# Kernel optimization log

Hardware: AMD Instinct MI355X
Metric: run time of the kernel (lower is better)

Reference implementation:

```python
import jax, jax.numpy as jnp
import numpy as np

EPS = 1e-6

def rmsnorm(x, w):
    rms = jnp.sqrt(jnp.mean(x * x, axis=-1, keepdims=True) + EPS)
    return w * x / rms

def setup_inputs() -> dict:
    key = jax.random.key(0)
    ks = jax.random.split(key, 12)
    B, L, D, S, E, H = 2, 2048, 1024, 16, 4, 2048
    x = jax.random.normal(ks[0], (B, L, D), jnp.float32)
    A_log = jnp.log(jax.random.uniform(ks[1], (D, S), jnp.float32) * 0.5 + 0.5)
    D_param = jnp.ones((D,), jnp.float32)
    W_delta = jax.random.normal(ks[2], (D, D), jnp.float32) * 0.02
    b_delta = jnp.zeros((D,), jnp.float32)
    W_B = jax.random.normal(ks[3], (D, S), jnp.float32) * 0.02
    W_C = jax.random.normal(ks[4], (D, S), jnp.float32) * 0.02
    W_router = jax.random.normal(ks[5], (D, E), jnp.float32) * 0.02
    Wg = jax.random.normal(ks[6], (E, D, H), jnp.float32) * 0.02
    Wu = jax.random.normal(ks[7], (E, D, H), jnp.float32) * 0.02
    Wd = jax.random.normal(ks[8], (E, H, D), jnp.float32) * 0.02
    wn_exp = jnp.ones((E, H), jnp.float32)
    norm_w = jnp.ones((D,), jnp.float32)
    return dict(x=x, A_log=A_log, D_param=D_param, W_delta=W_delta, b_delta=b_delta,
                W_B=W_B, W_C=W_C, W_router=W_router, Wg=Wg, Wu=Wu, Wd=Wd,
                wn_exp=wn_exp, norm_w=norm_w)

def reference(x, A_log, D_param, W_delta, b_delta, W_B, W_C, W_router, Wg, Wu, Wd, wn_exp, norm_w):
    B, L, D = x.shape
    # input-dependent SSM parameters
    delta = jax.nn.softplus(x @ W_delta + b_delta)        # (B,L,D)
    Bm = x @ W_B                                          # (B,L,S)
    Cm = x @ W_C                                          # (B,L,S)
    A = -jnp.exp(A_log)                                   # (D,S)
    S = A.shape[1]
    h0 = jnp.zeros((B, D, S), x.dtype)
    xs = (jnp.moveaxis(x, 1, 0), jnp.moveaxis(delta, 1, 0),
          jnp.moveaxis(Bm, 1, 0), jnp.moveaxis(Cm, 1, 0))

    def step(h, inp):
        x_t, d_t, B_t, C_t = inp                          # (B,D),(B,D),(B,S),(B,S)
        bar_A = jnp.exp(jnp.minimum(d_t[..., None] * A, 10.0))          # (B,D,S)
        bar_B = jnp.clip(d_t[..., None] * B_t[:, None, :], -10.0, 10.0)  # (B,D,S)
        h = jnp.clip(bar_A * h + bar_B * x_t[..., None], -10000.0, 10000.0)
        y_t = jnp.sum(h * C_t[:, None, :], axis=-1) + x_t * D_param     # (B,D)
        return h, y_t

    _, ys = jax.lax.scan(step, h0, xs)                    # ys: (L,B,D)
    ssm_out = jnp.moveaxis(ys, 0, 1)                      # (B,L,D)

    # top-2 MoE over flattened tokens
    flat = ssm_out.reshape(-1, D)                         # (N,D)
    probs = jax.nn.softmax(flat @ W_router, axis=-1)      # (N,E)
    w2, idx2 = jax.lax.top_k(probs, 2)
    w2 = w2 / (jnp.sum(w2, axis=-1, keepdims=True) + 1e-9)

    def expert(xf, wg, wu, wd, wn):
        g = jax.nn.silu(xf @ wg) * (xf @ wu)
        g = rmsnorm(g, wn)
        return g @ wd

    all_out = jax.vmap(expert, in_axes=(None, 0, 0, 0, 0))(flat, Wg, Wu, Wd, wn_exp)  # (E,N,D)
    tok = jnp.arange(flat.shape[0])
    moe = (w2[:, 0, None] * all_out[idx2[:, 0], tok]
           + w2[:, 1, None] * all_out[idx2[:, 1], tok])   # (N,D)

    out = rmsnorm(ssm_out + moe.reshape(B, L, D), norm_w)
    return out  # dropout is identity in eval mode
```

## Files before the change

### kernel.cpp

```cpp
#include <hip/hip_runtime.h>
#include <hip/hip_bf16.h>


typedef __bf16 bfrag __attribute__((ext_vector_type(8)));
typedef float f32x4 __attribute__((ext_vector_type(4)));

constexpr int Ddim = 1024;
constexpr int Sdim = 16;
constexpr int Eexp = 4;
constexpr int Hdim = 2048;
constexpr int Lseq = 2048;
constexpr int Bb   = 2;
constexpr int Ntok = 4096;
constexpr int NC   = 32;
constexpr int CL   = 64;
constexpr int DG   = 64;

__device__ __forceinline__ float softplus_f(float z) {
  return z > 20.f ? z : log1pf(__expf(z));
}

__device__ __forceinline__ bfrag cvt8(float4 a, float4 b) {
  bfrag r;
  r[0] = (__bf16)a.x; r[1] = (__bf16)a.y; r[2] = (__bf16)a.z; r[3] = (__bf16)a.w;
  r[4] = (__bf16)b.x; r[5] = (__bf16)b.y; r[6] = (__bf16)b.z; r[7] = (__bf16)b.w;
  return r;
}

__device__ __forceinline__ void cvt8_split(float4 a, float4 b, bfrag& h, bfrag& l) {
  float v[8] = {a.x, a.y, a.z, a.w, b.x, b.y, b.z, b.w};
  #pragma unroll
  for (int k = 0; k < 8; k++) {
    __bf16 hh = (__bf16)v[k];
    h[k] = hh;
    l[k] = (__bf16)(v[k] - (float)hh);
  }
}

__global__ __launch_bounds__(256) void tr_cvt(const float* __restrict__ src,
                                              __bf16* __restrict__ dst,
                                              int R, int C) {
  __shared__ float tile[32][33];
  const size_t boff = (size_t)blockIdx.z * R * C;
  const int c0 = blockIdx.x * 32, r0 = blockIdx.y * 32;
  const int tx = threadIdx.x & 31, ty = threadIdx.x >> 5;
  #pragma unroll
  for (int i = 0; i < 4; i++)
    tile[ty + 8 * i][tx] = src[boff + (size_t)(r0 + ty + 8 * i) * C + c0 + tx];
  __syncthreads();
  #pragma unroll
  for (int i = 0; i < 4; i++)
    dst[boff + (size_t)(c0 + ty + 8 * i) * R + r0 + tx] = (__bf16)tile[tx][ty + 8 * i];
}

__global__ __launch_bounds__(256) void tr_split(const float* __restrict__ src,
                                                __bf16* __restrict__ dhi,
                                                __bf16* __restrict__ dlo,
                                                int R, int C) {
  __shared__ float tile[32][33];
  const size_t boff = (size_t)blockIdx.z * R * C;
  const int c0 = blockIdx.x * 32, r0 = blockIdx.y * 32;
  const int tx = threadIdx.x & 31, ty = threadIdx.x >> 5;
  #pragma unroll
  for (int i = 0; i < 4; i++)
    tile[ty + 8 * i][tx] = src[boff + (size_t)(r0 + ty + 8 * i) * C + c0 + tx];
  __syncthreads();
  #pragma unroll
  for (int i = 0; i < 4; i++) {
    float v = tile[tx][ty + 8 * i];
    __bf16 h = (__bf16)v;
    size_t idx = boff + (size_t)(c0 + ty + 8 * i) * R + r0 + tx;
    dhi[idx] = h;
    dlo[idx] = (__bf16)(v - (float)h);
  }
}

__global__ __launch_bounds__(256) void gemm_delta(
    const float* __restrict__ Amat, const __bf16* __restrict__ Bhi,
    const __bf16* __restrict__ Blo, const float* __restrict__ bias,
    float* __restrict__ outp) {
  const int n0 = blockIdx.x * 128;
  const int m0 = blockIdx.y * 128;
  const int t = threadIdx.x;
  const int lane = t & 63;
  const int w = t >> 6;
  const int wm = w >> 1, wn = w & 1;
  const int lr = lane & 15, kq = lane >> 4;
  const int ar = t >> 1;
  const int ac = (t & 1) * 16;

  __shared__ __attribute__((aligned(16))) __bf16 Ah[128 * 48];
  __shared__ __attribute__((aligned(16))) __bf16 Alo[128 * 48];
  __shared__ __attribute__((aligned(16))) __bf16 Bh[128 * 48];
  __shared__ __attribute__((aligned(16))) __bf16 Bl[128 * 48];

  f32x4 acc[4][4];
  const f32x4 z4 = {0.f, 0.f, 0.f, 0.f};
  #pragma unroll
  for (int i = 0; i < 4; i++)
    #pragma unroll
    for (int j = 0; j < 4; j++) acc[i][j] = z4;

  const float* Asrc = Amat + (size_t)(m0 + ar) * Ddim + ac;
  const __bf16* Bhsrc = Bhi + (size_t)(n0 + ar) * Ddim + ac;
  const __bf16* Blsrc = Blo + (size_t)(n0 + ar) * Ddim + ac;

  for (int k0 = 0; k0 < Ddim; k0 += 32) {
    __syncthreads();
    {
      float4 f0 = *(const float4*)(Asrc + k0);
      float4 f1 = *(const float4*)(Asrc + k0 + 4);
      float4 f2 = *(const float4*)(Asrc + k0 + 8);
      float4 f3 = *(const float4*)(Asrc + k0 + 12);
      bfrag h0, l0, h1, l1;
      cvt8_split(f0, f1, h0, l0);
      cvt8_split(f2, f3, h1, l1);
      *(bfrag*)&Ah[ar * 48 + ac] = h0;
      *(bfrag*)&Ah[ar * 48 + ac + 8] = h1;
      *(bfrag*)&Alo[ar * 48 + ac] = l0;
      *(bfrag*)&Alo[ar * 48 + ac + 8] = l1;
      *(bfrag*)&Bh[ar * 48 + ac] = *(const bfrag*)(Bhsrc + k0);
      *(bfrag*)&Bh[ar * 48 + ac + 8] = *(const bfrag*)(Bhsrc + k0 + 8);
      *(bfrag*)&Bl[ar * 48 + ac] = *(const bfrag*)(Blsrc + k0);
      *(bfrag*)&Bl[ar * 48 + ac + 8] = *(const bfrag*)(Blsrc + k0 + 8);
    }
    __syncthreads();
    bfrag ah[4], al_[4], bh[4], bl[4];
    #pragma unroll
    for (int i = 0; i < 4; i++) {
      const int off = (wm * 64 + i * 16 + lr) * 48 + kq * 8;
      ah[i] = *(const bfrag*)&Ah[off];
      al_[i] = *(const bfrag*)&Alo[off];
    }
    #pragma unroll
    for (int j = 0; j < 4; j++) {
      const int off = (wn * 64 + j * 16 + lr) * 48 + kq * 8;
      bh[j] = *(const bfrag*)&Bh[off];
      bl[j] = *(const bfrag*)&Bl[off];
    }
    #pragma unroll
    for (int i = 0; i < 4; i++)
      #pragma unroll
      for (int j = 0; j < 4; j++) {
        f32x4 tacc = acc[i][j];
        tacc = __builtin_amdgcn_mfma_f32_16x16x32_bf16(al_[i], bl[j], tacc, 0, 0, 0);
        tacc = __builtin_amdgcn_mfma_f32_16x16x32_bf16(ah[i], bl[j], tacc, 0, 0, 0);
        tacc = __builtin_amdgcn_mfma_f32_16x16x32_bf16(al_[i], bh[j], tacc, 0, 0, 0);
        tacc = __builtin_amdgcn_mfma_f32_16x16x32_bf16(ah[i], bh[j], tacc, 0, 0, 0);
        acc[i][j] = tacc;
      }
  }
  #pragma unroll
  for (int i = 0; i < 4; i++)
    #pragma unroll
    for (int rr = 0; rr < 4; rr++) {
      const int row = m0 + wm * 64 + i * 16 + kq * 4 + rr;
      #pragma unroll
      for (int j = 0; j < 4; j++) {
        const int col = n0 + wn * 64 + j * 16 + lr;
        float zv = acc[i][j][rr] + bias[col];
        outp[(size_t)row * Ddim + col] = softplus_f(zv);
      }
    }
}

__global__ __launch_bounds__(256) void bc_proj(
    const float* __restrict__ x, const float* __restrict__ WB,
    const float* __restrict__ WC, float* __restrict__ Bm, float* __restrict__ Cm) {
  const int n = blockIdx.x * 4 + (threadIdx.x >> 6);
  const int lane = threadIdx.x & 63;
  const int o = lane & 31;
  const int half = lane >> 5;
  const int oc = o & 15;
  const float* W = (o < 16) ? WB : WC;
  const float* xr = x + (size_t)n * Ddim + half * 512;
  const float* Wp = W + (size_t)(half * 512) * Sdim + oc;
  float s = 0.f;
  #pragma unroll 8
  for (int k = 0; k < 512; k++) s += xr[k] * Wp[(size_t)k * Sdim];
  s += __shfl_xor(s, 32);
  if (half == 0) {
    if (o < 16) Bm[(size_t)n * Sdim + oc] = s;
    else        Cm[(size_t)n * Sdim + oc] = s;
  }
}

__global__ __launch_bounds__(1024) void scan_pass1(
    const float* __restrict__ delta, const float* __restrict__ x,
    const float* __restrict__ Bm, const float* __restrict__ A_log,
    float* __restrict__ Ac, float* __restrict__ Bc) {
  const int b = blockIdx.z, c = blockIdx.y, d0 = blockIdx.x * DG;
  const int tid = threadIdx.x;
  const int dl = tid >> 4, s = tid & 15;
  __shared__ __attribute__((aligned(16))) float ld[CL * DG];
  __shared__ __attribute__((aligned(16))) float lx[CL * DG];
  __shared__ __attribute__((aligned(16))) float lb[CL * 16];
  const int t0 = c * CL;
  {
    const int ti = tid >> 4, di = (tid & 15) * 4;
    const size_t src = ((size_t)(b * Lseq + t0 + ti)) * Ddim + d0 + di;
    *(float4*)&ld[ti * DG + di] = *(const float4*)&delta[src];
    *(float4*)&lx[ti * DG + di] = *(const float4*)&x[src];
    if (tid < 256) {
      const int tj = tid >> 2, sj = (tid & 3) * 4;
      *(float4*)&lb[tj * 16 + sj] =
          *(const float4*)&Bm[((size_t)(b * Lseq + t0 + tj)) * Sdim + sj];
    }
  }
  const float A = -__expf(A_log[(d0 + dl) * Sdim + s]);
  __syncthreads();
  float P = 1.f, S = 0.f;
  #pragma unroll 4
  for (int i = 0; i < CL; i++) {
    float dt = ld[i * DG + dl];
    float xt = lx[i * DG + dl];
    float Bt = lb[i * 16 + s];
    float a = __expf(fminf(dt * A, 10.f));
    float bb = fminf(fmaxf(dt * Bt, -10.f), 10.f);
    S = a * S + bb * xt;
    P *= a;
  }
  const size_t o = ((size_t)(b * NC + c) * Ddim + d0 + dl) * Sdim + s;
  Ac[o] = P;
  Bc[o] = S;
}

__global__ __launch_bounds__(256) void scan_pass2(float* __restrict__ Ac,
                                                  const float* __restrict__ Bc) {
  const int idx = blockIdx.x * 256 + threadIdx.x;
  const int b = idx >> 14, r = idx & 16383;
  const size_t base = (size_t)b * (NC * 16384) + r;
  float h = 0.f;
  #pragma unroll 4
  for (int c = 0; c < NC; c++) {
    const size_t a_idx = base + (size_t)c * 16384;
    float a = Ac[a_idx];
    float bb = Bc[a_idx];
    Ac[a_idx] = h;
    h = fmaf(a, h, bb);
  }
}

__global__ __launch_bounds__(1024) void scan_pass3(
    const float* __restrict__ delta, const float* __restrict__ x,
    const float* __restrict__ Bm, const float* __restrict__ Cm,
    const float* __restrict__ A_log, const float* __restrict__ Dp,
    const float* __restrict__ hstart, float* __restrict__ ssm) {
  const int b = blockIdx.z, c = blockIdx.y, d0 = blockIdx.x * DG;
  const int tid = threadIdx.x;
  const int dl = tid >> 4, s = tid & 15;
  __shared__ __attribute__((aligned(16))) float ld[CL * DG];
  __shared__ __attribute__((aligned(16))) float lx[CL * DG];
  __shared__ __attribute__((aligned(16))) float lb[CL * 16];
  __shared__ __attribute__((aligned(16))) float lc[CL * 16];
  __shared__ __attribute__((aligned(16))) float ly[CL * DG];
  const int t0 = c * CL;
  {
    const int ti = tid >> 4, di = (tid & 15) * 4;
    const size_t src = ((size_t)(b * Lseq + t0 + ti)) * Ddim + d0 + di;
    *(float4*)&ld[ti * DG + di] = *(const float4*)&delta[src];
    *(float4*)&lx[ti * DG + di] = *(const float4*)&x[src];
    if (tid < 256) {
      const int tj = tid >> 2, sj = (tid & 3) * 4;
      *(float4*)&lb[tj * 16 + sj] =
          *(const float4*)&Bm[((size_t)(b * Lseq + t0 + tj)) * Sdim + sj];
    } else if (tid < 512) {
      const int u = tid - 256;
      const int tj = u >> 2, sj = (u & 3) * 4;
      *(float4*)&lc[tj * 16 + sj] =
          *(const float4*)&Cm[((size_t)(b * Lseq + t0 + tj)) * Sdim + sj];
    }
  }
  const float A = -__expf(A_log[(d0 + dl) * Sdim + s]);
  const float Dpar = Dp[d0 + dl];
  float h = hstart[((size_t)(b * NC + c) * Ddim + d0 + dl) * Sdim + s];
  __syncthreads();
  #pragma unroll 2
  for (int i = 0; i < CL; i++) {
    float dt = ld[i * DG + dl];
    float xt = lx[i * DG + dl];
    float Bt = lb[i * 16 + s];
    float Ct = lc[i * 16 + s];
    float a = __expf(fminf(dt * A, 10.f));
    float bb = fminf(fmaxf(dt * Bt, -10.f), 10.f);
    h = a * h + bb * xt;
    float yp = h * Ct;
    yp += __shfl_xor(yp, 1);
    yp += __shfl_xor(yp, 2);
    yp += __shfl_xor(yp, 4);
    yp += __shfl_xor(yp, 8);
    if (s == 0) ly[i * DG + dl] = yp + xt * Dpar;
  }
  __syncthreads();
  {
    const int ti = tid >> 4, di = (tid & 15) * 4;
    *(float4*)&ssm[((size_t)(b * Lseq + t0 + ti)) * Ddim + d0 + di] =
        *(const float4*)&ly[ti * DG + di];
  }
}

__global__ __launch_bounds__(256) void router_k(
    const float* __restrict__ ssm, const float* __restrict__ Wr,
    int* __restrict__ counts, int* __restrict__ slotTok,
    int* __restrict__ tokSlot, float* __restrict__ tokW) {
  const int n = blockIdx.x * 4 + (threadIdx.x >> 6);
  const int lane = threadIdx.x & 63;
  const float* xr = ssm + (size_t)n * Ddim;
  float p0 = 0.f, p1 = 0.f, p2 = 0.f, p3 = 0.f;
  for (int k = lane; k < Ddim; k += 64) {
    float xv = xr[k];
    float4 wr = *(const float4*)&Wr[k * 4];
    p0 += xv * wr.x; p1 += xv * wr.y; p2 += xv * wr.z; p3 += xv * wr.w;
  }
  #pragma unroll
  for (int o = 32; o > 0; o >>= 1) {
    p0 += __shfl_xor(p0, o);
    p1 += __shfl_xor(p1, o);
    p2 += __shfl_xor(p2, o);
    p3 += __shfl_xor(p3, o);
  }
  if (lane == 0) {
    float l[4] = {p0, p1, p2, p3};
    float mx = fmaxf(fmaxf(l[0], l[1]), fmaxf(l[2], l[3]));
    float pe[4]; float sum = 0.f;
    #pragma unroll
    for (int e = 0; e < 4; e++) { pe[e] = __expf(l[e] - mx); sum += pe[e]; }
    int i0 = 0;
    #pragma unroll
    for (int e = 1; e < 4; e++) if (pe[e] > pe[i0]) i0 = e;
    int i1 = (i0 == 0) ? 1 : 0;
    #pragma unroll
    for (int e = 0; e < 4; e++) if (e != i0 && e != i1 && pe[e] > pe[i1]) i1 = e;
    float w0 = pe[i0] / sum, w1 = pe[i1] / sum;
    float dn = w0 + w1 + 1e-9f;
    w0 /= dn; w1 /= dn;
    int s0 = atomicAdd(&counts[i0], 1);
    slotTok[i0 * Ntok + s0] = n;
    tokSlot[2 * n] = i0 * Ntok + s0;
    tokW[2 * n] = w0;
    int s1 = atomicAdd(&counts[i1], 1);
    slotTok[i1 * Ntok + s1] = n;
    tokSlot[2 * n + 1] = i1 * Ntok + s1;
    tokW[2 * n + 1] = w1;
  }
}

__global__ void offs_k(const int* __restrict__ counts, int* __restrict__ offs) {
  if (threadIdx.x == 0 && blockIdx.x == 0) {
    int a = 0;
    for (int e = 0; e < Eexp; e++) { offs[e] = a; a += counts[e]; }
    offs[Eexp] = a;
  }
}

__global__ __launch_bounds__(256) void gemm_gateup(
    const float* __restrict__ ssm, const __bf16* __restrict__ WgT,
    const __bf16* __restrict__ WuT, const int* __restrict__ slotTok,
    const int* __restrict__ counts, const int* __restrict__ offs,
    __bf16* __restrict__ g) {
  const int e = blockIdx.z;
  const int cnt = counts[e];
  const int r0 = blockIdx.y * 128;
  if (r0 >= cnt) return;
  const int n0 = blockIdx.x * 128;
  const int t = threadIdx.x;
  const int lane = t & 63;
  const int w = t >> 6;
  const int wm = w >> 1, wn = w & 1;
  const int lr = lane & 15, kq = lane >> 4;
  const int ar = t >> 1;
  const int ac = (t & 1) * 16;

  __shared__ __attribute__((aligned(16))) __bf16 Al[128 * 48];
  __shared__ __attribute__((aligned(16))) __bf16 Bgl[128 * 48];
  __shared__ __attribute__((aligned(16))) __bf16 Bul[128 * 48];

  f32x4 accG[4][4], accU[4][4];
  const f32x4 z4 = {0.f, 0.f, 0.f, 0.f};
  #pragma unroll
  for (int i = 0; i < 4; i++)
    #pragma unroll
    for (int j = 0; j < 4; j++) { accG[i][j] = z4; accU[i][j] = z4; }

  const int rA = r0 + ar;
  const bool valid = rA < cnt;
  const int tok = valid ? slotTok[e * Ntok + rA] : 0;
  const float* Asrc = ssm + (size_t)tok * Ddim + ac;
  const __bf16* Bgsrc = WgT + (size_t)e * Hdim * Ddim + (size_t)(n0 + ar) * Ddim + ac;
  const __bf16* Busrc = WuT + (size_t)e * Hdim * Ddim + (size_t)(n0 + ar) * Ddim + ac;

  for (int k0 = 0; k0 < Ddim; k0 += 32) {
    __syncthreads();
    {
      bfrag v0, v1;
      if (valid) {
        float4 f0 = *(const float4*)(Asrc + k0);
        float4 f1 = *(const float4*)(Asrc + k0 + 4);
        float4 f2 = *(const float4*)(Asrc + k0 + 8);
        float4 f3 = *(const float4*)(Asrc + k0 + 12);
        v0 = cvt8(f0, f1);
        v1 = cvt8(f2, f3);
      } else {
        #pragma unroll
        for (int k = 0; k < 8; k++) { v0[k] = (__bf16)0.f; v1[k] = (__bf16)0.f; }
      }
      *(bfrag*)&Al[ar * 48 + ac] = v0;
      *(bfrag*)&Al[ar * 48 + ac + 8] = v1;
      *(bfrag*)&Bgl[ar * 48 + ac] = *(const bfrag*)(Bgsrc + k0);
      *(bfrag*)&Bgl[ar * 48 + ac + 8] = *(const bfrag*)(Bgsrc + k0 + 8);
      *(bfrag*)&Bul[ar * 48 + ac] = *(const bfrag*)(Busrc + k0);
      *(bfrag*)&Bul[ar * 48 + ac + 8] = *(const bfrag*)(Busrc + k0 + 8);
    }
    __syncthreads();
    bfrag af[4], bg[4], bu[4];
    #pragma unroll
    for (int i = 0; i < 4; i++) af[i] = *(const bfrag*)&Al[(wm * 64 + i * 16 + lr) * 48 + kq * 8];
    #pragma unroll
    for (int j = 0; j < 4; j++) {
      const int off = (wn * 64 + j * 16 + lr) * 48 + kq * 8;
      bg[j] = *(const bfrag*)&Bgl[off];
      bu[j] = *(const bfrag*)&Bul[off];
    }
    #pragma unroll
    for (int i = 0; i < 4; i++)
      #pragma unroll
      for (int j = 0; j < 4; j++) {
        accG[i][j] = __builtin_amdgcn_mfma_f32_16x16x32_bf16(af[i], bg[j], accG[i][j], 0, 0, 0);
        accU[i][j] = __builtin_amdgcn_mfma_f32_16x16x32_bf16(af[i], bu[j], accU[i][j], 0, 0, 0);
      }
  }
  const int gb = offs[e];
  #pragma unroll
  for (int i = 0; i < 4; i++)
    #pragma unroll
    for (int rr = 0; rr < 4; rr++) {
      const int r = r0 + wm * 64 + i * 16 + kq * 4 + rr;
      if (r < cnt) {
        const size_t base = (size_t)(gb + r) * Hdim + n0 + wn * 64 + lr;
        #pragma unroll
        for (int j = 0; j < 4; j++) {
          float zg = accG[i][j][rr];
          float zu = accU[i][j][rr];
          float val = zg / (1.f + __expf(-zg)) * zu;
          g[base + j * 16] = (__bf16)val;
        }
      }
    }
}

__global__ __launch_bounds__(256) void rms_g(__bf16* __restrict__ g,
                                             const float* __restrict__ wn,
                                             const int* __restrict__ offs) {
  const int gs = blockIdx.x;
  const int e = (gs >= offs[1]) + (gs >= offs[2]) + (gs >= offs[3]);
  __bf16* row = g + (size_t)gs * Hdim;
  const int t = threadIdx.x;
  bfrag v = *(const bfrag*)&row[t * 8];
  float f[8]; float ss = 0.f;
  #pragma unroll
  for (int k = 0; k < 8; k++) { f[k] = (float)v[k]; ss += f[k] * f[k]; }
  #pragma unroll
  for (int o = 32; o > 0; o >>= 1) ss += __shfl_xor(ss, o);
  __shared__ float red[4];
  if ((t & 63) == 0) red[t >> 6] = ss;
  __syncthreads();
  float tot = red[0] + red[1] + red[2] + red[3];
  float rinv = 1.f / sqrtf(tot * (1.f / Hdim) + 1e-6f);
  const float* wrow = wn + (size_t)e * Hdim + t * 8;
  bfrag o8;
  #pragma unroll
  for (int k = 0; k < 8; k++) o8[k] = (__bf16)(wrow[k] * f[k] * rinv);
  *(bfrag*)&row[t * 8] = o8;
}

__global__ __launch_bounds__(256) void gemm_down(
    const __bf16* __restrict__ g, const __bf16* __restrict__ WdT,
    const int* __restrict__ counts, const int* __restrict__ offs,
    float* __restrict__ dout) {
  const int e = blockIdx.z;
  const int cnt = counts[e];
  const int r0 = blockIdx.y * 128;
  if (r0 >= cnt) return;
  const int n0 = blockIdx.x * 128;
  const int t = threadIdx.x;
  const int lane = t & 63;
  const int w = t >> 6;
  const int wm = w >> 1, wn = w & 1;
  const int lr = lane & 15, kq = lane >> 4;
  const int ar = t >> 1;
  const int ac = (t & 1) * 16;

  __shared__ __attribute__((aligned(16))) __bf16 Al[128 * 48];
  __shared__ __attribute__((aligned(16))) __bf16 Bl[128 * 48];

  f32x4 acc[4][4];
  const f32x4 z4 = {0.f, 0.f, 0.f, 0.f};
  #pragma unroll
  for (int i = 0; i < 4; i++)
    #pragma unroll
    for (int j = 0; j < 4; j++) acc[i][j] = z4;

  const int rA = r0 + ar;
  const bool valid = rA < cnt;
  const __bf16* Asrc = g + ((size_t)offs[e] + (valid ? rA : 0)) * Hdim + ac;
  const __bf16* Bsrc = WdT + (size_t)e * Ddim * Hdim + (size_t)(n0 + ar) * Hdim + ac;

  for (int k0 = 0; k0 < Hdim; k0 += 32) {
    __syncthreads();
    *(bfrag*)&Al[ar * 48 + ac] = *(const bfrag*)(Asrc + k0);
    *(bfrag*)&Al[ar * 48 + ac + 8] = *(const bfrag*)(Asrc + k0 + 8);
    *(bfrag*)&Bl[ar * 48 + ac] = *(const bfrag*)(Bsrc + k0);
    *(bfrag*)&Bl[ar * 48 + ac + 8] = *(const bfrag*)(Bsrc + k0 + 8);
    __syncthreads();
    bfrag af[4], bf_[4];
    #pragma unroll
    for (int i = 0; i < 4; i++) af[i] = *(const bfrag*)&Al[(wm * 64 + i * 16 + lr) * 48 + kq * 8];
    #pragma unroll
    for (int j = 0; j < 4; j++) bf_[j] = *(const bfrag*)&Bl[(wn * 64 + j * 16 + lr) * 48 + kq * 8];
    #pragma unroll
    for (int i = 0; i < 4; i++)
      #pragma unroll
      for (int j = 0; j < 4; j++)
        acc[i][j] = __builtin_amdgcn_mfma_f32_16x16x32_bf16(af[i], bf_[j], acc[i][j], 0, 0, 0);
  }
  const int gb = offs[e];
  #pragma unroll
  for (int i = 0; i < 4; i++)
    #pragma unroll
    for (int rr = 0; rr < 4; rr++) {
      const int r = r0 + wm * 64 + i * 16 + kq * 4 + rr;
      if (r < cnt) {
        const size_t base = (size_t)(gb + r) * Ddim + n0 + wn * 64 + lr;
        #pragma unroll
        for (int j = 0; j < 4; j++)
          dout[base + j * 16] = acc[i][j][rr];
      }
    }
}

__global__ __launch_bounds__(256) void final_norm(
    const float* __restrict__ ssm, const float* __restrict__ dout,
    const int* __restrict__ tokSlot, const float* __restrict__ tokW,
    const int* __restrict__ offs, const float* __restrict__ nw,
    float* __restrict__ outp) {
  const int n = blockIdx.x;
  const int t = threadIdx.x;
  __shared__ int rows[2];
  __shared__ float ws[2];
  if (t < 2) {
    int pk = tokSlot[2 * n + t];
    rows[t] = offs[pk >> 12] + (pk & (Ntok - 1));
    ws[t] = tokW[2 * n + t];
  }
  __syncthreads();
  const int r0 = rows[0], r1 = rows[1];
  const float w0 = ws[0], w1 = ws[1];
  const size_t base = (size_t)n * Ddim + t * 4;
  float4 a = *(const float4*)&ssm[base];
  float4 m0 = *(const float4*)&dout[(size_t)r0 * Ddim + t * 4];
  float4 m1 = *(const float4*)&dout[(size_t)r1 * Ddim + t * 4];
  float v0 = a.x + w0 * m0.x + w1 * m1.x;
  float v1 = a.y + w0 * m0.y + w1 * m1.y;
  float v2 = a.z + w0 * m0.z + w1 * m1.z;
  float v3 = a.w + w0 * m0.w + w1 * m1.w;
  float ss = v0 * v0 + v1 * v1 + v2 * v2 + v3 * v3;
  #pragma unroll
  for (int o = 32; o > 0; o >>= 1) ss += __shfl_xor(ss, o);
  __shared__ float red[4];
  if ((t & 63) == 0) red[t >> 6] = ss;
  __syncthreads();
  float tot = red[0] + red[1] + red[2] + red[3];
  float rinv = 1.f / sqrtf(tot * (1.f / Ddim) + 1e-6f);
  float4 wv = *(const float4*)&nw[t * 4];
  float4 r;
  r.x = wv.x * v0 * rinv;
  r.y = wv.y * v1 * rinv;
  r.z = wv.z * v2 * rinv;
  r.w = wv.w * v3 * rinv;
  *(float4*)&outp[base] = r;
}

extern "C" void kernel_launch(void* const* d_in, const int* in_sizes, int n_in,
                              void* d_out, int out_size, void* d_ws, size_t ws_size,
                              hipStream_t stream) {
  (void)in_sizes; (void)n_in; (void)out_size; (void)ws_size;
  const float* x        = (const float*)d_in[0];
  const float* A_log    = (const float*)d_in[1];
  const float* D_param  = (const float*)d_in[2];
  const float* W_delta  = (const float*)d_in[3];
  const float* b_delta  = (const float*)d_in[4];
  const float* W_B      = (const float*)d_in[5];
  const float* W_C      = (const float*)d_in[6];
  const float* W_router = (const float*)d_in[7];
  const float* Wg       = (const float*)d_in[8];
  const float* Wu       = (const float*)d_in[9];
  const float* Wd       = (const float*)d_in[10];
  const float* wn_exp   = (const float*)d_in[11];
  const float* norm_w   = (const float*)d_in[12];
  float* out = (float*)d_out;

  char* p = (char*)d_ws;
  auto carve = [&](size_t bytes) -> void* {
    void* r = (void*)p;
    p += (bytes + 255) & ~(size_t)255;
    return r;
  };
  float*  delta   = (float*)  carve((size_t)Ntok * Ddim * 4);
  float*  Ac      = (float*)  carve((size_t)Bb * NC * Ddim * Sdim * 4);
  float*  Bc      = (float*)  carve((size_t)Bb * NC * Ddim * Sdim * 4);
  __bf16* WdT_hi  = (__bf16*) carve((size_t)Ddim * Ddim * 2);
  __bf16* WdT_lo  = (__bf16*) carve((size_t)Ddim * Ddim * 2);
  __bf16* WgT     = (__bf16*) carve((size_t)Eexp * Hdim * Ddim * 2);
  float*  dout    = delta;
  __bf16* WuT     = (__bf16*) carve((size_t)Eexp * Hdim * Ddim * 2);
  __bf16* WdnT    = (__bf16*) carve((size_t)Eexp * Ddim * Hdim * 2);
  float*  Bm      = (float*)  carve((size_t)Ntok * Sdim * 4);
  float*  Cm      = (float*)  carve((size_t)Ntok * Sdim * 4);
  float*  ssm     = (float*)  carve((size_t)Ntok * Ddim * 4);
  __bf16* gbuf    = (__bf16*) carve((size_t)2 * Ntok * Hdim * 2);
  int*    counts  = (int*)    carve(64);
  int*    offs    = (int*)    carve(64);
  int*    slotTok = (int*)    carve((size_t)Eexp * Ntok * 4);
  int*    tokSlot = (int*)    carve((size_t)2 * Ntok * 4);
  float*  tokW    = (float*)  carve((size_t)2 * Ntok * 4);

  hipMemsetAsync(counts, 0, 64, stream);

  tr_split<<<dim3(Ddim / 32, Ddim / 32, 1), 256, 0, stream>>>(W_delta, WdT_hi, WdT_lo, Ddim, Ddim);
  tr_cvt<<<dim3(Hdim / 32, Ddim / 32, Eexp), 256, 0, stream>>>(Wg, WgT, Ddim, Hdim);
  tr_cvt<<<dim3(Hdim / 32, Ddim / 32, Eexp), 256, 0, stream>>>(Wu, WuT, Ddim, Hdim);
  tr_cvt<<<dim3(Ddim / 32, Hdim / 32, Eexp), 256, 0, stream>>>(Wd, WdnT, Hdim, Ddim);

  gemm_delta<<<dim3(Ddim / 128, Ntok / 128), 256, 0, stream>>>(x, WdT_hi, WdT_lo, b_delta, delta);
  bc_proj<<<Ntok / 4, 256, 0, stream>>>(x, W_B, W_C, Bm, Cm);

  scan_pass1<<<dim3(Ddim / DG, NC, Bb), 1024, 0, stream>>>(delta, x, Bm, A_log, Ac, Bc);
  scan_pass2<<<Bb * Ddim * Sdim / 256, 256, 0, stream>>>(Ac, Bc);
  scan_pass3<<<dim3(Ddim / DG, NC, Bb), 1024, 0, stream>>>(delta, x, Bm, Cm, A_log, D_param, Ac, ssm);

  router_k<<<Ntok / 4, 256, 0, stream>>>(ssm, W_router, counts, slotTok, tokSlot, tokW);
  offs_k<<<1, 64, 0, stream>>>(counts, offs);
  gemm_gateup<<<dim3(Hdim / 128, Ntok / 128, Eexp), 256, 0, stream>>>(ssm, WgT, WuT, slotTok, counts, offs, gbuf);
  rms_g<<<2 * Ntok, 256, 0, stream>>>(gbuf, wn_exp, offs);
  gemm_down<<<dim3(Ddim / 128, Ntok / 128, Eexp), 256, 0, stream>>>(gbuf, WdnT, counts, offs, dout);
  final_norm<<<Ntok, 256, 0, stream>>>(ssm, dout, tokSlot, tokW, offs, norm_w, out);
}
```

Measured before the change: 795.1 us.

## Pre-convert GEMM activations to bf16 and stage tiles with direct global-to-LDS loads

Three MFMA GEMMs (delta projection, expert gate/up, expert down) now fill shared memory with global_load_lds 16-byte transfers instead of loading into registers and storing to LDS. To make that possible, new elementwise kernels convert x (into hi/lo bf16 parts) and the SSM output to bf16 ahead of time, so the GEMMs no longer convert fp32 inside their inner loops. Scratch buffers (Ac, gbuf, delta) are reused to hold the converted data. The unpadded 32-element LDS rows may cause bank conflicts on the fragment reads, and the extra conversion passes add memory traffic.

```diff
diff --git a/kernel.cpp b/kernel.cpp
--- a/kernel.cpp
+++ b/kernel.cpp
@@ -37,6 +37,12 @@
   }
 }
 
+__device__ __forceinline__ void gload16(const void* g, void* l) {
+  __builtin_amdgcn_global_load_lds(
+      (const __attribute__((address_space(1))) void*)g,
+      (__attribute__((address_space(3))) void*)l, 16, 0, 0);
+}
+
 __global__ __launch_bounds__(256) void tr_cvt(const float* __restrict__ src,
                                               __bf16* __restrict__ dst,
                                               int R, int C) {
@@ -75,10 +81,30 @@
   }
 }
 
+__global__ __launch_bounds__(256) void cvt_bf(const float* __restrict__ s,
+                                              __bf16* __restrict__ d) {
+  const size_t i = ((size_t)blockIdx.x * 256 + threadIdx.x) * 8;
+  float4 f0 = *(const float4*)&s[i];
+  float4 f1 = *(const float4*)&s[i + 4];
+  *(bfrag*)&d[i] = cvt8(f0, f1);
+}
+
+__global__ __launch_bounds__(256) void cvt_xsplit(const float* __restrict__ s,
+                                                  __bf16* __restrict__ dh,
+                                                  __bf16* __restrict__ dl) {
+  const size_t i = ((size_t)blockIdx.x * 256 + threadIdx.x) * 8;
+  float4 f0 = *(const float4*)&s[i];
+  float4 f1 = *(const float4*)&s[i + 4];
+  bfrag h, l;
+  cvt8_split(f0, f1, h, l);
+  *(bfrag*)&dh[i] = h;
+  *(bfrag*)&dl[i] = l;
+}
+
 __global__ __launch_bounds__(256) void gemm_delta(
-    const float* __restrict__ Amat, const __bf16* __restrict__ Bhi,
-    const __bf16* __restrict__ Blo, const float* __restrict__ bias,
-    float* __restrict__ outp) {
+    const __bf16* __restrict__ xh, const __bf16* __restrict__ xl,
+    const __bf16* __restrict__ Bhi, const __bf16* __restrict__ Blo,
+    const float* __restrict__ bias, float* __restrict__ outp) {
   const int n0 = blockIdx.x * 128;
   const int m0 = blockIdx.y * 128;
   const int t = threadIdx.x;
@@ -86,13 +112,11 @@
   const int w = t >> 6;
   const int wm = w >> 1, wn = w & 1;
   const int lr = lane & 15, kq = lane >> 4;
-  const int ar = t >> 1;
-  const int ac = (t & 1) * 16;
-
-  __shared__ __attribute__((aligned(16))) __bf16 Ah[128 * 48];
-  __shared__ __attribute__((aligned(16))) __bf16 Alo[128 * 48];
-  __shared__ __attribute__((aligned(16))) __bf16 Bh[128 * 48];
-  __shared__ __attribute__((aligned(16))) __bf16 Bl[128 * 48];
+
+  __shared__ __attribute__((aligned(16))) __bf16 Ah[128 * 32];
+  __shared__ __attribute__((aligned(16))) __bf16 Al[128 * 32];
+  __shared__ __attribute__((aligned(16))) __bf16 Bh[128 * 32];
+  __shared__ __attribute__((aligned(16))) __bf16 Bl[128 * 32];
 
   f32x4 acc[4][4];
   const f32x4 z4 = {0.f, 0.f, 0.f, 0.f};
@@ -101,40 +125,43 @@
     #pragma unroll
     for (int j = 0; j < 4; j++) acc[i][j] = z4;
 
-  const float* Asrc = Amat + (size_t)(m0 + ar) * Ddim + ac;
-  const __bf16* Bhsrc = Bhi + (size_t)(n0 + ar) * Ddim + ac;
-  const __bf16* Blsrc = Blo + (size_t)(n0 + ar) * Ddim + ac;
+  const int sr0 = (w * 2 + 0) * 16 + (lane >> 2);
+  const int sr1 = (w * 2 + 1) * 16 + (lane >> 2);
+  const int skc = (lane & 3) * 8;
+  const __bf16* ah0 = xh + (size_t)(m0 + sr0) * Ddim + skc;
+  const __bf16* ah1 = xh + (size_t)(m0 + sr1) * Ddim + skc;
+  const __bf16* al0 = xl + (size_t)(m0 + sr0) * Ddim + skc;
+  const __bf16* al1 = xl + (size_t)(m0 + sr1) * Ddim + skc;
+  const __bf16* bh0 = Bhi + (size_t)(n0 + sr0) * Ddim + skc;
+  const __bf16* bh1 = Bhi + (size_t)(n0 + sr1) * Ddim + skc;
+  const __bf16* bl0 = Blo + (size_t)(n0 + sr0) * Ddim + skc;
+  const __bf16* bl1 = Blo + (size_t)(n0 + sr1) * Ddim + skc;
+  __bf16* lAh0 = &Ah[(w * 2 + 0) * 512];
+  __bf16* lAh1 = &Ah[(w * 2 + 1) * 512];
+  __bf16* lAl0 = &Al[(w * 2 + 0) * 512];
+  __bf16* lAl1 = &Al[(w * 2 + 1) * 512];
+  __bf16* lBh0 = &Bh[(w * 2 + 0) * 512];
+  __bf16* lBh1 = &Bh[(w * 2 + 1) * 512];
+  __bf16* lBl0 = &Bl[(w * 2 + 0) * 512];
+  __bf16* lBl1 = &Bl[(w * 2 + 1) * 512];
 
   for (int k0 = 0; k0 < Ddim; k0 += 32) {
     __syncthreads();
-    {
-      float4 f0 = *(const float4*)(Asrc + k0);
-      float4 f1 = *(const float4*)(Asrc + k0 + 4);
-      float4 f2 = *(const float4*)(Asrc + k0 + 8);
-      float4 f3 = *(const float4*)(Asrc + k0 + 12);
-      bfrag h0, l0, h1, l1;
-      cvt8_split(f0, f1, h0, l0);
-      cvt8_split(f2, f3, h1, l1);
-      *(bfrag*)&Ah[ar * 48 + ac] = h0;
-      *(bfrag*)&Ah[ar * 48 + ac + 8] = h1;
-      *(bfrag*)&Alo[ar * 48 + ac] = l0;
-      *(bfrag*)&Alo[ar * 48 + ac + 8] = l1;
-      *(bfrag*)&Bh[ar * 48 + ac] = *(const bfrag*)(Bhsrc + k0);
-      *(bfrag*)&Bh[ar * 48 + ac + 8] = *(const bfrag*)(Bhsrc + k0 + 8);
-      *(bfrag*)&Bl[ar * 48 + ac] = *(const bfrag*)(Blsrc + k0);
-      *(bfrag*)&Bl[ar * 48 + ac + 8] = *(const bfrag*)(Blsrc + k0 + 8);
-    }
+    gload16(ah0 + k0, lAh0); gload16(ah1 + k0, lAh1);
+    gload16(al0 + k0, lAl0); gload16(al1 + k0, lAl1);
+    gload16(bh0 + k0, lBh0); gload16(bh1 + k0, lBh1);
+    gload16(bl0 + k0, lBl0); gload16(bl1 + k0, lBl1);
     __syncthreads();
     bfrag ah[4], al_[4], bh[4], bl[4];
     #pragma unroll
     for (int i = 0; i < 4; i++) {
-      const int off = (wm * 64 + i * 16 + lr) * 48 + kq * 8;
+      const int off = (wm * 64 + i * 16 + lr) * 32 + kq * 8;
       ah[i] = *(const bfrag*)&Ah[off];
-      al_[i] = *(const bfrag*)&Alo[off];
+      al_[i] = *(const bfrag*)&Al[off];
     }
     #pragma unroll
     for (int j = 0; j < 4; j++) {
-      const int off = (wn * 64 + j * 16 + lr) * 48 + kq * 8;
+      const int off = (wn * 64 + j * 16 + lr) * 32 + kq * 8;
       bh[j] = *(const bfrag*)&Bh[off];
       bl[j] = *(const bfrag*)&Bl[off];
     }
@@ -354,7 +381,7 @@
 }
 
 __global__ __launch_bounds__(256) void gemm_gateup(
-    const float* __restrict__ ssm, const __bf16* __restrict__ WgT,
+    const __bf16* __restrict__ ssmB, const __bf16* __restrict__ WgT,
     const __bf16* __restrict__ WuT, const int* __restrict__ slotTok,
     const int* __restrict__ counts, const int* __restrict__ offs,
     __bf16* __restrict__ g) {
@@ -368,12 +395,10 @@
   const int w = t >> 6;
   const int wm = w >> 1, wn = w & 1;
   const int lr = lane & 15, kq = lane >> 4;
-  const int ar = t >> 1;
-  const int ac = (t & 1) * 16;
-
-  __shared__ __attribute__((aligned(16))) __bf16 Al[128 * 48];
-  __shared__ __attribute__((aligned(16))) __bf16 Bgl[128 * 48];
-  __shared__ __attribute__((aligned(16))) __bf16 Bul[128 * 48];
+
+  __shared__ __attribute__((aligned(16))) __bf16 As[128 * 32];
+  __shared__ __attribute__((aligned(16))) __bf16 Bgs[128 * 32];
+  __shared__ __attribute__((aligned(16))) __bf16 Bus[128 * 32];
 
   f32x4 accG[4][4], accU[4][4];
   const f32x4 z4 = {0.f, 0.f, 0.f, 0.f};
@@ -382,44 +407,40 @@
     #pragma unroll
     for (int j = 0; j < 4; j++) { accG[i][j] = z4; accU[i][j] = z4; }
 
-  const int rA = r0 + ar;
-  const bool valid = rA < cnt;
-  const int tok = valid ? slotTok[e * Ntok + rA] : 0;
-  const float* Asrc = ssm + (size_t)tok * Ddim + ac;
-  const __bf16* Bgsrc = WgT + (size_t)e * Hdim * Ddim + (size_t)(n0 + ar) * Ddim + ac;
-  const __bf16* Busrc = WuT + (size_t)e * Hdim * Ddim + (size_t)(n0 + ar) * Ddim + ac;
+  const int sr0 = (w * 2 + 0) * 16 + (lane >> 2);
+  const int sr1 = (w * 2 + 1) * 16 + (lane >> 2);
+  const int skc = (lane & 3) * 8;
+  const int ra0 = (r0 + sr0 < cnt) ? (r0 + sr0) : (cnt - 1);
+  const int ra1 = (r0 + sr1 < cnt) ? (r0 + sr1) : (cnt - 1);
+  const __bf16* a0 = ssmB + (size_t)slotTok[e * Ntok + ra0] * Ddim + skc;
+  const __bf16* a1 = ssmB + (size_t)slotTok[e * Ntok + ra1] * Ddim + skc;
+  const size_t wb = (size_t)e * Hdim * Ddim;
+  const __bf16* bg0 = WgT + wb + (size_t)(n0 + sr0) * Ddim + skc;
+  const __bf16* bg1 = WgT + wb + (size_t)(n0 + sr1) * Ddim + skc;
+  const __bf16* bu0 = WuT + wb + (size_t)(n0 + sr0) * Ddim + skc;
+  const __bf16* bu1 = WuT + wb + (size_t)(n0 + sr1) * Ddim + skc;
+  __bf16* lA0 = &As[(w * 2 + 0) * 512];
+  __bf16* lA1 = &As[(w * 2 + 1) * 512];
+  __bf16* lBg0 = &Bgs[(w * 2 + 0) * 512];
+  __bf16* lBg1 = &Bgs[(w * 2 + 1) * 512];
+  __bf16* lBu0 = &Bus[(w * 2 + 0) * 512];
+  __bf16* lBu1 = &Bus[(w * 2 + 1) * 512];
 
   for (int k0 = 0; k0 < Ddim; k0 += 32) {
     __syncthreads();
-    {
-      bfrag v0, v1;
-      if (valid) {
-        float4 f0 = *(const float4*)(Asrc + k0);
-        float4 f1 = *(const float4*)(Asrc + k0 + 4);
-        float4 f2 = *(const float4*)(Asrc + k0 + 8);
-        float4 f3 = *(const float4*)(Asrc + k0 + 12);
-        v0 = cvt8(f0, f1);
-        v1 = cvt8(f2, f3);
-      } else {
-        #pragma unroll
-        for (int k = 0; k < 8; k++) { v0[k] = (__bf16)0.f; v1[k] = (__bf16)0.f; }
-      }
-      *(bfrag*)&Al[ar * 48 + ac] = v0;
-      *(bfrag*)&Al[ar * 48 + ac + 8] = v1;
-      *(bfrag*)&Bgl[ar * 48 + ac] = *(const bfrag*)(Bgsrc + k0);
-      *(bfrag*)&Bgl[ar * 48 + ac + 8] = *(const bfrag*)(Bgsrc + k0 + 8);
-      *(bfrag*)&Bul[ar * 48 + ac] = *(const bfrag*)(Busrc + k0);
-      *(bfrag*)&Bul[ar * 48 + ac + 8] = *(const bfrag*)(Busrc + k0 + 8);
-    }
+    gload16(a0 + k0, lA0);  gload16(a1 + k0, lA1);
+    gload16(bg0 + k0, lBg0); gload16(bg1 + k0, lBg1);
+    gload16(bu0 + k0, lBu0); gload16(bu1 + k0, lBu1);
     __syncthreads();
     bfrag af[4], bg[4], bu[4];
     #pragma unroll
-    for (int i = 0; i < 4; i++) af[i] = *(const bfrag*)&Al[(wm * 64 + i * 16 + lr) * 48 + kq * 8];
+    for (int i = 0; i < 4; i++)
+      af[i] = *(const bfrag*)&As[(wm * 64 + i * 16 + lr) * 32 + kq * 8];
     #pragma unroll
     for (int j = 0; j < 4; j++) {
-      const int off = (wn * 64 + j * 16 + lr) * 48 + kq * 8;
-      bg[j] = *(const bfrag*)&Bgl[off];
-      bu[j] = *(const bfrag*)&Bul[off];
+      const int off = (wn * 64 + j * 16 + lr) * 32 + kq * 8;
+      bg[j] = *(const bfrag*)&Bgs[off];
+      bu[j] = *(const bfrag*)&Bus[off];
     }
     #pragma unroll
     for (int i = 0; i < 4; i++)
@@ -487,11 +508,9 @@
   const int w = t >> 6;
   const int wm = w >> 1, wn = w & 1;
   const int lr = lane & 15, kq = lane >> 4;
-  const int ar = t >> 1;
-  const int ac = (t & 1) * 16;
-
-  __shared__ __attribute__((aligned(16))) __bf16 Al[128 * 48];
-  __shared__ __attribute__((aligned(16))) __bf16 Bl[128 * 48];
+
+  __shared__ __attribute__((aligned(16))) __bf16 As[128 * 32];
+  __shared__ __attribute__((aligned(16))) __bf16 Bs[128 * 32];
 
   f32x4 acc[4][4];
   const f32x4 z4 = {0.f, 0.f, 0.f, 0.f};
@@ -500,30 +519,40 @@
     #pragma unroll
     for (int j = 0; j < 4; j++) acc[i][j] = z4;
 
-  const int rA = r0 + ar;
-  const bool valid = rA < cnt;
-  const __bf16* Asrc = g + ((size_t)offs[e] + (valid ? rA : 0)) * Hdim + ac;
-  const __bf16* Bsrc = WdT + (size_t)e * Ddim * Hdim + (size_t)(n0 + ar) * Hdim + ac;
+  const int sr0 = (w * 2 + 0) * 16 + (lane >> 2);
+  const int sr1 = (w * 2 + 1) * 16 + (lane >> 2);
+  const int skc = (lane & 3) * 8;
+  const int gb = offs[e];
+  const int ra0 = (r0 + sr0 < cnt) ? (r0 + sr0) : (cnt - 1);
+  const int ra1 = (r0 + sr1 < cnt) ? (r0 + sr1) : (cnt - 1);
+  const __bf16* a0 = g + (size_t)(gb + ra0) * Hdim + skc;
+  const __bf16* a1 = g + (size_t)(gb + ra1) * Hdim + skc;
+  const size_t wb = (size_t)e * Ddim * Hdim;
+  const __bf16* b0 = WdT + wb + (size_t)(n0 + sr0) * Hdim + skc;
+  const __bf16* b1 = WdT + wb + (size_t)(n0 + sr1) * Hdim + skc;
+  __bf16* lA0 = &As[(w * 2 + 0) * 512];
+  __bf16* lA1 = &As[(w * 2 + 1) * 512];
+  __bf16* lB0 = &Bs[(w * 2 + 0) * 512];
+  __bf16* lB1 = &Bs[(w * 2 + 1) * 512];
 
   for (int k0 = 0; k0 < Hdim; k0 += 32) {
     __syncthreads();
-    *(bfrag*)&Al[ar * 48 + ac] = *(const bfrag*)(Asrc + k0);
-    *(bfrag*)&Al[ar * 48 + ac + 8] = *(const bfrag*)(Asrc + k0 + 8);
-    *(bfrag*)&Bl[ar * 48 + ac] = *(const bfrag*)(Bsrc + k0);
-    *(bfrag*)&Bl[ar * 48 + ac + 8] = *(const bfrag*)(Bsrc + k0 + 8);
+    gload16(a0 + k0, lA0); gload16(a1 + k0, lA1);
+    gload16(b0 + k0, lB0); gload16(b1 + k0, lB1);
     __syncthreads();
     bfrag af[4], bf_[4];
     #pragma unroll
-    for (int i = 0; i < 4; i++) af[i] = *(const bfrag*)&Al[(wm * 64 + i * 16 + lr) * 48 + kq * 8];
-    #pragma unroll
-    for (int j = 0; j < 4; j++) bf_[j] = *(const bfrag*)&Bl[(wn * 64 + j * 16 + lr) * 48 + kq * 8];
+    for (int i = 0; i < 4; i++)
+      af[i] = *(const bfrag*)&As[(wm * 64 + i * 16 + lr) * 32 + kq * 8];
+    #pragma unroll
+    for (int j = 0; j < 4; j++)
+      bf_[j] = *(const bfrag*)&Bs[(wn * 64 + j * 16 + lr) * 32 + kq * 8];
     #pragma unroll
     for (int i = 0; i < 4; i++)
       #pragma unroll
       for (int j = 0; j < 4; j++)
         acc[i][j] = __builtin_amdgcn_mfma_f32_16x16x32_bf16(af[i], bf_[j], acc[i][j], 0, 0, 0);
   }
-  const int gb = offs[e];
   #pragma unroll
   for (int i = 0; i < 4; i++)
     #pragma unroll
@@ -624,6 +653,10 @@
   int*    tokSlot = (int*)    carve((size_t)2 * Ntok * 4);
   float*  tokW    = (float*)  carve((size_t)2 * Ntok * 4);
 
+  __bf16* xh   = (__bf16*)Ac;
+  __bf16* xl   = (__bf16*)gbuf;
+  __bf16* ssmB = (__bf16*)delta;
+
   hipMemsetAsync(counts, 0, 64, stream);
 
   tr_split<<<dim3(Ddim / 32, Ddim / 32, 1), 256, 0, stream>>>(W_delta, WdT_hi, WdT_lo, Ddim, Ddim);
@@ -631,16 +664,18 @@
   tr_cvt<<<dim3(Hdim / 32, Ddim / 32, Eexp), 256, 0, stream>>>(Wu, WuT, Ddim, Hdim);
   tr_cvt<<<dim3(Ddim / 32, Hdim / 32, Eexp), 256, 0, stream>>>(Wd, WdnT, Hdim, Ddim);
 
-  gemm_delta<<<dim3(Ddim / 128, Ntok / 128), 256, 0, stream>>>(x, WdT_hi, WdT_lo, b_delta, delta);
+  cvt_xsplit<<<Ntok * Ddim / 2048, 256, 0, stream>>>(x, xh, xl);
+  gemm_delta<<<dim3(Ddim / 128, Ntok / 128), 256, 0, stream>>>(xh, xl, WdT_hi, WdT_lo, b_delta, delta);
   bc_proj<<<Ntok / 4, 256, 0, stream>>>(x, W_B, W_C, Bm, Cm);
 
   scan_pass1<<<dim3(Ddim / DG, NC, Bb), 1024, 0, stream>>>(delta, x, Bm, A_log, Ac, Bc);
   scan_pass2<<<Bb * Ddim * Sdim / 256, 256, 0, stream>>>(Ac, Bc);
   scan_pass3<<<dim3(Ddim / DG, NC, Bb), 1024, 0, stream>>>(delta, x, Bm, Cm, A_log, D_param, Ac, ssm);
 
+  cvt_bf<<<Ntok * Ddim / 2048, 256, 0, stream>>>(ssm, ssmB);
   router_k<<<Ntok / 4, 256, 0, stream>>>(ssm, W_router, counts, slotTok, tokSlot, tokW);
   offs_k<<<1, 64, 0, stream>>>(counts, offs);
-  gemm_gateup<<<dim3(Hdim / 128, Ntok / 128, Eexp), 256, 0, stream>>>(ssm, WgT, WuT, slotTok, counts, offs, gbuf);
+  gemm_gateup<<<dim3(Hdim / 128, Ntok / 128, Eexp), 256, 0, stream>>>(ssmB, WgT, WuT, slotTok, counts, offs, gbuf);
   rms_g<<<2 * Ntok, 256, 0, stream>>>(gbuf, wn_exp, offs);
   gemm_down<<<dim3(Ddim / 128, Ntok / 128, Eexp), 256, 0, stream>>>(gbuf, WdnT, counts, offs, dout);
   final_norm<<<Ntok, 256, 0, stream>>>(ssm, dout, tokSlot, tokW, offs, norm_w, out);
```

New measurement: 789.5 us. About the same (-0.7%).
